# Kernel optimization log

Measured on AMD Instinct MI355X. Metric: run time of the kernel, lower is better.

Reference implementation:

```python
import jax, jax.numpy as jnp
import numpy as np

N_NODES = 100000
N_EDGES = 1600000
N_FEAT = 8
N_EFEAT = 4
STATE = 32  # node_state_size
N_GEN = 10000
ITERS = 3


def _fix_max(m):
    # TF unsorted_segment_max fills empty segments with dtype.min (finite)
    return jnp.where(jnp.isneginf(m), jnp.finfo(m.dtype).min, m)


def _fix_min(m):
    return jnp.where(jnp.isposinf(m), jnp.finfo(m.dtype).max, m)


def _l2_normalize(x, eps=1e-12):
    return x * jax.lax.rsqrt(jnp.maximum(jnp.sum(x * x, axis=-1, keepdims=True), eps))


def _dense_init(key, fan_in, fan_out):
    return jax.random.normal(key, (fan_in, fan_out), jnp.float32) * (1.0 / np.sqrt(fan_in))


def setup_inputs() -> dict:
    key = jax.random.key(0)
    ks = jax.random.split(key, 12)
    x = jax.random.normal(ks[0], (N_NODES, N_FEAT), jnp.float32)
    edge_weights = jax.random.uniform(ks[1], (N_EDGES, N_EFEAT), jnp.float32)
    edges = jax.random.randint(ks[2], (2, N_EDGES), 0, N_NODES)
    generators_nodes = jax.random.randint(ks[3], (N_GEN,), 0, N_NODES)
    # update_fn: 128 -> 256 -> 128 -> 32 (tanh)
    Wu1 = _dense_init(ks[4], 4 * STATE, 256); bu1 = jnp.zeros((256,), jnp.float32)
    Wu2 = _dense_init(ks[5], 256, 128);       bu2 = jnp.zeros((128,), jnp.float32)
    Wu3 = _dense_init(ks[6], 128, STATE);     bu3 = jnp.zeros((STATE,), jnp.float32)
    # readout: 32 -> 64 -> 32 -> 1 (tanh, tanh, linear)
    Wr1 = _dense_init(ks[7], STATE, 64);      br1 = jnp.zeros((64,), jnp.float32)
    Wr2 = _dense_init(ks[8], 64, 32);         br2 = jnp.zeros((32,), jnp.float32)
    Wr3 = _dense_init(ks[9], 32, 1);          br3 = jnp.zeros((1,), jnp.float32)
    return {"x": x, "edge_weights": edge_weights,
            "Wu1": Wu1, "bu1": bu1, "Wu2": Wu2, "bu2": bu2, "Wu3": Wu3, "bu3": bu3,
            "Wr1": Wr1, "br1": br1, "Wr2": Wr2, "br2": br2, "Wr3": Wr3, "br3": br3,
            "edges": edges, "generators_nodes": generators_nodes}


def reference(x, edge_weights, Wu1, bu1, Wu2, bu2, Wu3, bu3,
              Wr1, br1, Wr2, br2, Wr3, br3, edges, generators_nodes):
    n = x.shape[0]
    node_idx, nbr_idx = edges[0], edges[1]
    ones = jnp.ones((edge_weights.shape[0], 1), x.dtype)
    cnt = jnp.maximum(jax.ops.segment_sum(ones, node_idx, num_segments=n), 1.0)  # [n,1]

    # prepare(): edge-weight stats per destination node, concat with features, pad to STATE
    w_sum = jax.ops.segment_sum(edge_weights, node_idx, num_segments=n)
    w_mean = w_sum / cnt
    w_max = _fix_max(jax.ops.segment_max(edge_weights, node_idx, num_segments=n))
    w_min = _fix_min(jax.ops.segment_min(edge_weights, node_idx, num_segments=n))
    reps = jnp.concatenate([x, w_mean, w_max, w_min, w_sum], axis=1)  # [n, 24]
    reps = jnp.pad(reps, ((0, 0), (0, STATE - reps.shape[1])))        # [n, 32]

    for _ in range(ITERS):
        msgs = jnp.take(reps, nbr_idx, axis=0)  # gather neighbour states [E, 32]
        m_mean = jax.ops.segment_sum(msgs, node_idx, num_segments=n) / cnt
        m_max = _fix_max(jax.ops.segment_max(msgs, node_idx, num_segments=n))
        m_min = _fix_min(jax.ops.segment_min(msgs, node_idx, num_segments=n))
        h = jnp.concatenate([reps, m_mean, m_max, m_min], axis=1)  # [n, 128]
        h = jnp.tanh(h @ Wu1 + bu1)
        h = jnp.tanh(h @ Wu2 + bu2)
        h = jnp.tanh(h @ Wu3 + bu3)
        reps = _l2_normalize(h)

    reps = jnp.where(jnp.isnan(reps), jnp.zeros_like(reps), reps)
    g = jnp.take(reps, generators_nodes, axis=0)  # [n_gen, 32]
    g = jnp.tanh(g @ Wr1 + br1)
    g = jnp.tanh(g @ Wr2 + br2)
    values = g @ Wr3 + br3  # linear final activation
    return values.reshape(-1)
```

## Files before the change

### kernel.cpp

```cpp
#include <hip/hip_runtime.h>
#include <cfloat>
#include <cmath>


typedef _Float16 half_t;
typedef _Float16 half8 __attribute__((ext_vector_type(8)));
typedef _Float16 half4_t __attribute__((ext_vector_type(4)));
typedef _Float16 half2_t __attribute__((ext_vector_type(2)));
typedef float f32x4 __attribute__((ext_vector_type(4)));

#define NPB 512
#define BIN_CAP 9216
#define IDXCAP 4352

__device__ __forceinline__ float fast_tanh(float x) {
    float e = __builtin_amdgcn_exp2f(x * 2.8853900817779268f);
    return 1.0f - 2.0f * __builtin_amdgcn_rcpf(1.0f + e);
}

__device__ __forceinline__ half_t cvt_clamp(float v) {
    return (half_t)fminf(fmaxf(v, -60000.f), 60000.f);
}

__device__ __forceinline__ half2_t h2shfl_xor(half2_t v, int mask) {
    int i = __builtin_bit_cast(int, v);
    i = __shfl_xor(i, mask);
    return __builtin_bit_cast(half2_t, i);
}

__global__ __launch_bounds__(256) void k_binA(
    const int* __restrict__ dst, const int* __restrict__ src,
    const float4* __restrict__ ew4,
    int* __restrict__ binCnt, int4* __restrict__ staged, int E, int nbins) {
    __shared__ int cnt[256], base[256], cur[256];
    int t = threadIdx.x;
    cnt[t] = 0;
    cur[t] = 0;
    __syncthreads();
    int e0 = blockIdx.x * 8192;
#pragma unroll 4
    for (int i = 0; i < 32; ++i) {
        int e = e0 + i * 256 + t;
        if (e < E) atomicAdd(&cnt[dst[e] >> 9], 1);
    }
    __syncthreads();
    if (t < nbins && cnt[t] > 0) base[t] = atomicAdd(&binCnt[t], cnt[t]);
    __syncthreads();
#pragma unroll 4
    for (int i = 0; i < 32; ++i) {
        int e = e0 + i * 256 + t;
        if (e < E) {
            int d = dst[e];
            int b = d >> 9;
            int j = base[b] + atomicAdd(&cur[b], 1);
            if (j < BIN_CAP) {
                float4 w = ew4[e];
                half2_t lo = {(half_t)w.x, (half_t)w.y};
                half2_t hi = {(half_t)w.z, (half_t)w.w};
                staged[(size_t)b * BIN_CAP + j] =
                    make_int4(src[e], d & (NPB - 1),
                              __builtin_bit_cast(int, lo),
                              __builtin_bit_cast(int, hi));
            }
        }
    }
}

__global__ void k_scanN(const int* __restrict__ binCnt, int* __restrict__ binStart,
                        int* __restrict__ row_start, int nbins, int n, int E) {
    __shared__ int sh[256];
    int t = threadIdx.x;
    int v = (t < nbins) ? binCnt[t] : 0;
    sh[t] = v;
    __syncthreads();
    for (int s = 1; s < 256; s <<= 1) {
        int u = (t >= s) ? sh[t - s] : 0;
        __syncthreads();
        sh[t] += u;
        __syncthreads();
    }
    if (t < nbins) binStart[t] = sh[t] - v;
    if (t == 0) row_start[n] = E;
}

__global__ __launch_bounds__(512) void k_binB(
    const int* __restrict__ binCnt, const int* __restrict__ binStart,
    const int4* __restrict__ staged, const float* __restrict__ x,
    int* __restrict__ row_start, int* __restrict__ snbr, int2* __restrict__ sew,
    half_t* __restrict__ reps, int n) {
    __shared__ int deg[NPB], cur[NPB], rsl[NPB];
    int t = threadIdx.x;
    int bin = blockIdx.x;
    int cntE = min(binCnt[bin], BIN_CAP);
    int pbase = binStart[bin];
    const int4* st = staged + (size_t)bin * BIN_CAP;

    deg[t] = 0;
    cur[t] = 0;
    __syncthreads();

    for (int i = t; i < cntE; i += 512)
        atomicAdd(&deg[st[i].y], 1);
    __syncthreads();

    int own = deg[t];
    for (int s = 1; s < NPB; s <<= 1) {
        int u = (t >= s) ? deg[t - s] : 0;
        __syncthreads();
        deg[t] += u;
        __syncthreads();
    }
    int excl = deg[t] - own;
    rsl[t] = pbase + excl;
    int node = bin * NPB + t;
    if (node < n) row_start[node] = pbase + excl;
    __syncthreads();

    for (int i = t; i < cntE; i += 512) {
        int4 v = st[i];
        int p = rsl[v.y] + atomicAdd(&cur[v.y], 1);
        snbr[p] = v.x;
        sew[p] = make_int2(v.z, v.w);
    }
    __syncthreads();

    if (node < n) {
        int base = rsl[t];
        float s0 = 0.f, s1 = 0.f, s2 = 0.f, s3 = 0.f;
        half2_t mxlo = {(half_t)-65504.f, (half_t)-65504.f};
        half2_t mxhi = mxlo;
        half2_t mnlo = {(half_t)65504.f, (half_t)65504.f};
        half2_t mnhi = mnlo;
#pragma unroll 2
        for (int k = 0; k < own; ++k) {
            int2 e = sew[base + k];
            half2_t lo = __builtin_bit_cast(half2_t, e.x);
            half2_t hi = __builtin_bit_cast(half2_t, e.y);
            s0 += (float)lo[0];
            s1 += (float)lo[1];
            s2 += (float)hi[0];
            s3 += (float)hi[1];
            mxlo = __builtin_elementwise_max(mxlo, lo);
            mxhi = __builtin_elementwise_max(mxhi, hi);
            mnlo = __builtin_elementwise_min(mnlo, lo);
            mnhi = __builtin_elementwise_min(mnhi, hi);
        }
        float cnt = fmaxf((float)own, 1.0f);
        float rc = __builtin_amdgcn_rcpf(cnt);
        float mx0, mx1, mx2, mx3, mn0, mn1, mn2, mn3;
        if (own == 0) {
            mx0 = mx1 = mx2 = mx3 = -FLT_MAX;
            mn0 = mn1 = mn2 = mn3 = FLT_MAX;
        } else {
            mx0 = (float)mxlo[0]; mx1 = (float)mxlo[1];
            mx2 = (float)mxhi[0]; mx3 = (float)mxhi[1];
            mn0 = (float)mnlo[0]; mn1 = (float)mnlo[1];
            mn2 = (float)mnhi[0]; mn3 = (float)mnhi[1];
        }
        const float4* x4 = reinterpret_cast<const float4*>(x);
        float4 x0 = x4[node * 2 + 0], x1 = x4[node * 2 + 1];
        half_t* o = &reps[(size_t)node * 32];
        half8 c0 = {cvt_clamp(x0.x), cvt_clamp(x0.y), cvt_clamp(x0.z), cvt_clamp(x0.w),
                    cvt_clamp(x1.x), cvt_clamp(x1.y), cvt_clamp(x1.z), cvt_clamp(x1.w)};
        half8 c1 = {cvt_clamp(s0 * rc), cvt_clamp(s1 * rc), cvt_clamp(s2 * rc), cvt_clamp(s3 * rc),
                    cvt_clamp(mx0), cvt_clamp(mx1), cvt_clamp(mx2), cvt_clamp(mx3)};
        half8 c2 = {cvt_clamp(mn0), cvt_clamp(mn1), cvt_clamp(mn2), cvt_clamp(mn3),
                    cvt_clamp(s0), cvt_clamp(s1), cvt_clamp(s2), cvt_clamp(s3)};
        half8 c3 = {(half_t)0.f, (half_t)0.f, (half_t)0.f, (half_t)0.f,
                    (half_t)0.f, (half_t)0.f, (half_t)0.f, (half_t)0.f};
        *(half8*)&o[0] = c0;
        *(half8*)&o[8] = c1;
        *(half8*)&o[16] = c2;
        *(half8*)&o[24] = c3;
    }
}

__global__ void k_wprep(const float* __restrict__ Wu1, const float* __restrict__ Wu2,
                        const float* __restrict__ Wu3, half_t* __restrict__ Wt1,
                        half_t* __restrict__ Wt2, half_t* __restrict__ Wt3) {
    int i = blockIdx.x * 256 + threadIdx.x;
    if (i < 32768) {
        int nrow = i >> 7, k = i & 127;
        Wt1[i] = (half_t)Wu1[k * 256 + nrow];
    } else if (i < 65536) {
        int j = i - 32768;
        int nrow = j >> 8, k = j & 255;
        Wt2[j] = (half_t)Wu2[k * 128 + nrow];
    } else if (i < 69632) {
        int j = i - 65536;
        int nrow = j >> 7, k = j & 127;
        Wt3[j] = (half_t)Wu3[k * 32 + nrow];
    }
}

#define MFMA16(a, b, c) __builtin_amdgcn_mfma_f32_16x16x32_f16((a), (b), (c), 0, 0, 0)

__global__ __launch_bounds__(512, 6) void k_mlp(
    const half_t* __restrict__ reps_in,
    const int* __restrict__ row_start, const int* __restrict__ snbr,
    const int* __restrict__ nlist, int nlen,
    const half_t* __restrict__ Wt1, const half_t* __restrict__ Wt2,
    const half_t* __restrict__ Wt3,
    const float* __restrict__ bu1, const float* __restrict__ bu2,
    const float* __restrict__ bu3,
    half_t* __restrict__ reps_out, int n) {
    __shared__ half_t sH[64 * 136];
    __shared__ half_t sh1c[64 * 136];
    __shared__ int sDeg[64], sPerm[64], sNode[64];
    int* sIdx = (int*)sh1c;

    const int tid = threadIdx.x;
    const int w   = tid >> 6;
    const int l15 = tid & 15;
    const int lk  = (tid & 63) >> 4;
    const int node0 = blockIdx.x * 64;

    if (tid < 64) {
        int node;
        if (nlist) {
            int li = node0 + tid;
            node = (li < nlen) ? nlist[li] : -1;
        } else {
            node = node0 + tid;
        }
        if ((unsigned)node >= (unsigned)n) node = -1;
        sNode[tid] = node;
        sDeg[tid] = (node >= 0) ? (row_start[node + 1] - row_start[node]) : 0;
    }
    const int nodeEnd = min(node0 + 64, n);
    int d0blk = 0;
    bool lds_ok = false;
    if (!nlist && node0 < n) {
        d0blk = row_start[node0];
        int ecnt = row_start[nodeEnd] - d0blk;
        lds_ok = (ecnt <= IDXCAP);
        if (lds_ok) {
            for (int i = tid; i < ecnt; i += 512)
                sIdx[i] = __builtin_nontemporal_load(&snbr[d0blk + i]);
        }
    }
    __syncthreads();
    if (tid < 64) {
        int dg = sDeg[tid];
        int rank = 0;
#pragma unroll
        for (int j = 0; j < 64; ++j) {
            int dj = sDeg[j];
            rank += (dj > dg) || (dj == dg && j < tid);
        }
        sPerm[rank] = tid;
    }
    __syncthreads();

    {
        const int sg = tid >> 4;
        const int l  = tid & 15;
        const int nb = l >> 2;
        const int ch = l & 3;

        for (int i = 0; i < 2; ++i) {
            int nl = sPerm[i * 32 + sg];
            int node = sNode[nl];
            float s[8];
            half2_t mx2[4], mn2[4];
#pragma unroll
            for (int f = 0; f < 8; ++f) s[f] = 0.f;
#pragma unroll
            for (int f = 0; f < 4; ++f) {
                mx2[f] = (half2_t){(half_t)-65504.f, (half_t)-65504.f};
                mn2[f] = (half2_t){(half_t)65504.f, (half_t)65504.f};
            }
            int d0 = 0, d1 = 0;
            if (node >= 0) { d0 = row_start[node]; d1 = row_start[node + 1]; }

            for (int e = d0; e < d1; e += 16) {
                int e0 = e + nb, e1 = e + 4 + nb, e2 = e + 8 + nb, e3 = e + 12 + nb;
                float m0 = (e0 < d1) ? 1.f : 0.f;
                float m1 = (e1 < d1) ? 1.f : 0.f;
                float m2 = (e2 < d1) ? 1.f : 0.f;
                float m3 = (e3 < d1) ? 1.f : 0.f;
                int ii0, ii1, ii2, ii3;
                if (lds_ok) {
                    ii0 = sIdx[min(e0, d1 - 1) - d0blk];
                    ii1 = sIdx[min(e1, d1 - 1) - d0blk];
                    ii2 = sIdx[min(e2, d1 - 1) - d0blk];
                    ii3 = sIdx[min(e3, d1 - 1) - d0blk];
                } else {
                    ii0 = snbr[min(e0, d1 - 1)];
                    ii1 = snbr[min(e1, d1 - 1)];
                    ii2 = snbr[min(e2, d1 - 1)];
                    ii3 = snbr[min(e3, d1 - 1)];
                }
                half8 r0 = *(const half8*)&reps_in[(size_t)ii0 * 32 + ch * 8];
                half8 r1 = *(const half8*)&reps_in[(size_t)ii1 * 32 + ch * 8];
                half8 r2 = *(const half8*)&reps_in[(size_t)ii2 * 32 + ch * 8];
                half8 r3 = *(const half8*)&reps_in[(size_t)ii3 * 32 + ch * 8];
#pragma unroll
                for (int f = 0; f < 4; ++f) {
                    half2_t a0 = (half2_t){r0[2 * f], r0[2 * f + 1]};
                    half2_t a1 = (half2_t){r1[2 * f], r1[2 * f + 1]};
                    half2_t a2 = (half2_t){r2[2 * f], r2[2 * f + 1]};
                    half2_t a3 = (half2_t){r3[2 * f], r3[2 * f + 1]};
                    mx2[f] = __builtin_elementwise_max(
                        __builtin_elementwise_max(mx2[f], a0),
                        __builtin_elementwise_max(a1,
                            __builtin_elementwise_max(a2, a3)));
                    mn2[f] = __builtin_elementwise_min(
                        __builtin_elementwise_min(mn2[f], a0),
                        __builtin_elementwise_min(a1,
                            __builtin_elementwise_min(a2, a3)));
                }
#pragma unroll
                for (int f = 0; f < 8; ++f) {
                    s[f] = fmaf((float)r0[f], m0, s[f]);
                    s[f] = fmaf((float)r1[f], m1, s[f]);
                    s[f] = fmaf((float)r2[f], m2, s[f]);
                    s[f] = fmaf((float)r3[f], m3, s[f]);
                }
            }
#pragma unroll
            for (int f = 0; f < 8; ++f) {
                s[f] += __shfl_xor(s[f], 4);
                s[f] += __shfl_xor(s[f], 8);
            }
#pragma unroll
            for (int f = 0; f < 4; ++f) {
                mx2[f] = __builtin_elementwise_max(mx2[f], h2shfl_xor(mx2[f], 4));
                mx2[f] = __builtin_elementwise_max(mx2[f], h2shfl_xor(mx2[f], 8));
                mn2[f] = __builtin_elementwise_min(mn2[f], h2shfl_xor(mn2[f], 4));
                mn2[f] = __builtin_elementwise_min(mn2[f], h2shfl_xor(mn2[f], 8));
            }
            float cnt = fmaxf((float)(d1 - d0), 1.f);
            half8 o;
            if (nb == 0) {
                if (node >= 0) {
                    o = *(const half8*)&reps_in[(size_t)node * 32 + ch * 8];
                } else {
#pragma unroll
                    for (int f = 0; f < 8; ++f) o[f] = (half_t)0.f;
                }
            } else if (nb == 1) {
                float rc = __builtin_amdgcn_rcpf(cnt);
#pragma unroll
                for (int f = 0; f < 8; ++f) o[f] = cvt_clamp(s[f] * rc);
            } else if (nb == 2) {
#pragma unroll
                for (int f = 0; f < 4; ++f) {
                    o[2 * f]     = cvt_clamp((float)mx2[f][0]);
                    o[2 * f + 1] = cvt_clamp((float)mx2[f][1]);
                }
            } else {
#pragma unroll
                for (int f = 0; f < 4; ++f) {
                    o[2 * f]     = cvt_clamp((float)mn2[f][0]);
                    o[2 * f + 1] = cvt_clamp((float)mn2[f][1]);
                }
            }
            *(half8*)&sH[nl * 136 + l * 8] = o;
        }
    }
    __syncthreads();

    f32x4 acc2[4] = {{0.f, 0.f, 0.f, 0.f}, {0.f, 0.f, 0.f, 0.f},
                     {0.f, 0.f, 0.f, 0.f}, {0.f, 0.f, 0.f, 0.f}};
#pragma unroll
    for (int c = 0; c < 2; ++c) {
        {
            half8 a[4];
#pragma unroll
            for (int ks = 0; ks < 4; ++ks)
                a[ks] = *(const half8*)&Wt1[(c * 128 + w * 16 + l15) * 128 + ks * 32 + lk * 8];
            f32x4 bv = *(const f32x4*)&bu1[c * 128 + w * 16 + lk * 4];
#pragma unroll
            for (int nt = 0; nt < 4; ++nt) {
                const half_t* hrow = &sH[(nt * 16 + l15) * 136 + lk * 8];
                half8 b0 = *(const half8*)&hrow[0];
                half8 b1 = *(const half8*)&hrow[32];
                half8 b2 = *(const half8*)&hrow[64];
                half8 b3 = *(const half8*)&hrow[96];
                f32x4 acc = {0.f, 0.f, 0.f, 0.f};
                acc = MFMA16(a[0], b0, acc);
                acc = MFMA16(a[1], b1, acc);
                acc = MFMA16(a[2], b2, acc);
                acc = MFMA16(a[3], b3, acc);
                half4_t o;
#pragma unroll
                for (int r = 0; r < 4; ++r)
                    o[r] = (half_t)fast_tanh(acc[r] + bv[r]);
                *(half4_t*)&sh1c[(nt * 16 + l15) * 136 + w * 16 + lk * 4] = o;
            }
        }
        __syncthreads();
        {
            half8 a[4];
#pragma unroll
            for (int ks = 0; ks < 4; ++ks)
                a[ks] = *(const half8*)&Wt2[(w * 16 + l15) * 256 + c * 128 + ks * 32 + lk * 8];
#pragma unroll
            for (int nt = 0; nt < 4; ++nt) {
#pragma unroll
                for (int ks = 0; ks < 4; ++ks) {
                    half8 b = *(const half8*)&sh1c[(nt * 16 + l15) * 136 + ks * 32 + lk * 8];
                    acc2[nt] = MFMA16(a[ks], b, acc2[nt]);
                }
            }
        }
        __syncthreads();
    }

    {
        f32x4 bv = *(const f32x4*)&bu2[w * 16 + lk * 4];
#pragma unroll
        for (int nt = 0; nt < 4; ++nt) {
            half4_t o;
#pragma unroll
            for (int r = 0; r < 4; ++r)
                o[r] = (half_t)fast_tanh(acc2[nt][r] + bv[r]);
            *(half4_t*)&sH[(nt * 16 + l15) * 136 + w * 16 + lk * 4] = o;
        }
    }
    __syncthreads();

    if (w < 4) {
        half8 a0[4], a1[4], b[4];
#pragma unroll
        for (int ks = 0; ks < 4; ++ks) {
            a0[ks] = *(const half8*)&Wt3[l15 * 128 + ks * 32 + lk * 8];
            a1[ks] = *(const half8*)&Wt3[(16 + l15) * 128 + ks * 32 + lk * 8];
            b[ks]  = *(const half8*)&sH[(w * 16 + l15) * 136 + ks * 32 + lk * 8];
        }
        f32x4 acc0 = {0.f, 0.f, 0.f, 0.f}, acc1 = {0.f, 0.f, 0.f, 0.f};
#pragma unroll
        for (int ks = 0; ks < 4; ++ks) {
            acc0 = MFMA16(a0[ks], b[ks], acc0);
            acc1 = MFMA16(a1[ks], b[ks], acc1);
        }
        f32x4 bv0 = *(const f32x4*)&bu3[lk * 4];
        f32x4 bv1 = *(const f32x4*)&bu3[16 + lk * 4];
        float v0[4], v1[4];
        float ss = 0.f;
#pragma unroll
        for (int r = 0; r < 4; ++r) {
            v0[r] = fast_tanh(acc0[r] + bv0[r]);
            v1[r] = fast_tanh(acc1[r] + bv1[r]);
            ss += v0[r] * v0[r] + v1[r] * v1[r];
        }
        ss += __shfl_xor(ss, 16);
        ss += __shfl_xor(ss, 32);
        float sc = rsqrtf(fmaxf(ss, 1e-12f));
        int node = sNode[w * 16 + l15];
        if (node >= 0) {
            half4_t o0, o1;
#pragma unroll
            for (int r = 0; r < 4; ++r) {
                o0[r] = (half_t)(v0[r] * sc);
                o1[r] = (half_t)(v1[r] * sc);
            }
            *(half4_t*)&reps_out[(size_t)node * 32 + lk * 4] = o0;
            *(half4_t*)&reps_out[(size_t)node * 32 + 16 + lk * 4] = o1;
        }
    }
}

__global__ __launch_bounds__(256) void k_readout(
    const half_t* __restrict__ reps, const int* __restrict__ gen,
    const float* __restrict__ Wr1, const float* __restrict__ br1,
    const float* __restrict__ Wr2, const float* __restrict__ br2,
    const float* __restrict__ Wr3, const float* __restrict__ br3,
    float* __restrict__ out, int ngen) {
    __shared__ float sW1[32 * 64];
    __shared__ float sW2[64 * 32];
    __shared__ float sb1[64];
    __shared__ float sb2[32];
    __shared__ float sW3r[32];
    __shared__ float sb3;
    int tid = threadIdx.x;
    for (int i = tid; i < 2048; i += 256) sW1[i] = Wr1[i];
    for (int i = tid; i < 2048; i += 256) sW2[i] = Wr2[i];
    if (tid < 64) sb1[tid] = br1[tid];
    if (tid < 32) sb2[tid] = br2[tid];
    if (tid < 32) sW3r[tid] = Wr3[tid];
    if (tid == 0) sb3 = br3[0];
    __syncthreads();
    int ig = blockIdx.x * 256 + tid;
    if (ig >= ngen) return;
    int node = gen[ig];
    float g[32];
#pragma unroll
    for (int q = 0; q < 4; ++q) {
        half8 v = *(const half8*)&reps[(size_t)node * 32 + q * 8];
#pragma unroll
        for (int r = 0; r < 8; ++r) {
            float f = (float)v[r];
            g[q * 8 + r] = (f != f) ? 0.f : f;
        }
    }
    float a[64];
#pragma unroll
    for (int o = 0; o < 64; ++o) {
        float acc = sb1[o];
#pragma unroll
        for (int k = 0; k < 32; ++k) acc = fmaf(g[k], sW1[k * 64 + o], acc);
        a[o] = fast_tanh(acc);
    }
    float b[32];
#pragma unroll
    for (int o = 0; o < 32; ++o) {
        float acc = sb2[o];
#pragma unroll
        for (int k = 0; k < 64; ++k) acc = fmaf(a[k], sW2[k * 32 + o], acc);
        b[o] = fast_tanh(acc);
    }
    float acc = sb3;
#pragma unroll
    for (int k = 0; k < 32; ++k) acc = fmaf(b[k], sW3r[k], acc);
    out[ig] = acc;
}

extern "C" void kernel_launch(void* const* d_in, const int* in_sizes, int n_in,
                              void* d_out, int out_size, void* d_ws, size_t ws_size,
                              hipStream_t stream) {
    const float* x   = (const float*)d_in[0];
    const float* ew  = (const float*)d_in[1];
    const float* Wu1 = (const float*)d_in[2];
    const float* bu1 = (const float*)d_in[3];
    const float* Wu2 = (const float*)d_in[4];
    const float* bu2 = (const float*)d_in[5];
    const float* Wu3 = (const float*)d_in[6];
    const float* bu3 = (const float*)d_in[7];
    const float* Wr1 = (const float*)d_in[8];
    const float* br1 = (const float*)d_in[9];
    const float* Wr2 = (const float*)d_in[10];
    const float* br2 = (const float*)d_in[11];
    const float* Wr3 = (const float*)d_in[12];
    const float* br3 = (const float*)d_in[13];
    const int* edges = (const int*)d_in[14];
    const int* gen   = (const int*)d_in[15];

    const int n    = in_sizes[0] / 8;
    const int E    = in_sizes[1] / 4;
    const int ngen = in_sizes[15];
    const int* dst = edges;
    const int* src = edges + E;
    float* out = (float*)d_out;

    const int nblk  = (n + 63) / 64;
    const int npad  = nblk * 64;
    const int nbins = (n + NPB - 1) / NPB;

    char* ws = (char*)d_ws;
    size_t off = 0;
    auto alloc = [&](size_t bytes) -> char* {
        char* p = ws + off;
        off = (off + bytes + 255) & ~(size_t)255;
        return p;
    };
    int* row_start = (int*)alloc((size_t)(n + 1) * 4);
    int* binCnt    = (int*)alloc(256 * 4);
    int* binStart  = (int*)alloc(256 * 4);
    int* snbr      = (int*)alloc((size_t)E * 4);
    int2* sew      = (int2*)alloc((size_t)E * 8);
    half_t* repsA  = (half_t*)alloc((size_t)npad * 32 * 2);
    half_t* repsB  = (half_t*)alloc((size_t)npad * 32 * 2);
    half_t* Wt1    = (half_t*)alloc(32768 * 2);
    half_t* Wt2    = (half_t*)alloc(32768 * 2);
    half_t* Wt3    = (half_t*)alloc(4096 * 2);
    int4* staged   = (int4*)alloc((size_t)nbins * BIN_CAP * 16);

    hipMemsetAsync(binCnt, 0, 256 * 4, stream);
    int nblkA = (E + 8191) / 8192;
    k_binA<<<nblkA, 256, 0, stream>>>(dst, src, (const float4*)ew, binCnt, staged, E, nbins);
    k_scanN<<<1, 256, 0, stream>>>(binCnt, binStart, row_start, nbins, n, E);
    k_binB<<<nbins, 512, 0, stream>>>(binCnt, binStart, staged, x,
                                      row_start, snbr, sew, repsA, n);
    k_wprep<<<272, 256, 0, stream>>>(Wu1, Wu2, Wu3, Wt1, Wt2, Wt3);

    k_mlp<<<nblk, 512, 0, stream>>>(repsA, row_start, snbr, nullptr, 0,
                                    Wt1, Wt2, Wt3, bu1, bu2, bu3, repsB, n);
    k_mlp<<<nblk, 512, 0, stream>>>(repsB, row_start, snbr, nullptr, 0,
                                    Wt1, Wt2, Wt3, bu1, bu2, bu3, repsA, n);
    int nblk3 = (ngen + 63) / 64;
    k_mlp<<<nblk3, 512, 0, stream>>>(repsA, row_start, snbr, gen, ngen,
                                     Wt1, Wt2, Wt3, bu1, bu2, bu3, repsB, n);

    k_readout<<<(ngen + 255) / 256, 256, 0, stream>>>(repsB, gen, Wr1, br1, Wr2, br2,
                                                      Wr3, br3, out, ngen);
}
```

Measured before the change: 261.8 us.

## Halve k_mlp node tile to 32 with 256-thread blocks and 2x MFMA tiles per wave

Shrinks each k_mlp block from 64 nodes/512 threads to 32 nodes/256 threads, halving shared-memory buffers and the LDS index cap. Each of the four waves now computes two 16-row output tiles per layer, so weight fragments are loaded twice per wave while per-block node work halves. The aim is more, smaller blocks for better load balance and occupancy, at the cost of reloading weights from global/L2 for twice as many blocks.

```diff
diff --git a/kernel.cpp b/kernel.cpp
--- a/kernel.cpp
+++ b/kernel.cpp
@@ -11,7 +11,7 @@
 
 #define NPB 512
 #define BIN_CAP 9216
-#define IDXCAP 4352
+#define IDXCAP 2176
 
 __device__ __forceinline__ float fast_tanh(float x) {
     float e = __builtin_amdgcn_exp2f(x * 2.8853900817779268f);
@@ -195,7 +195,7 @@
 
 #define MFMA16(a, b, c) __builtin_amdgcn_mfma_f32_16x16x32_f16((a), (b), (c), 0, 0, 0)
 
-__global__ __launch_bounds__(512, 6) void k_mlp(
+__global__ __launch_bounds__(256, 6) void k_mlp(
     const half_t* __restrict__ reps_in,
     const int* __restrict__ row_start, const int* __restrict__ snbr,
     const int* __restrict__ nlist, int nlen,
@@ -204,18 +204,18 @@
     const float* __restrict__ bu1, const float* __restrict__ bu2,
     const float* __restrict__ bu3,
     half_t* __restrict__ reps_out, int n) {
-    __shared__ half_t sH[64 * 136];
-    __shared__ half_t sh1c[64 * 136];
-    __shared__ int sDeg[64], sPerm[64], sNode[64];
+    __shared__ half_t sH[32 * 136];
+    __shared__ half_t sh1c[32 * 136];
+    __shared__ int sDeg[32], sPerm[32], sNode[32];
     int* sIdx = (int*)sh1c;
 
     const int tid = threadIdx.x;
     const int w   = tid >> 6;
     const int l15 = tid & 15;
     const int lk  = (tid & 63) >> 4;
-    const int node0 = blockIdx.x * 64;
-
-    if (tid < 64) {
+    const int node0 = blockIdx.x * 32;
+
+    if (tid < 32) {
         int node;
         if (nlist) {
             int li = node0 + tid;
@@ -227,7 +227,7 @@
         sNode[tid] = node;
         sDeg[tid] = (node >= 0) ? (row_start[node + 1] - row_start[node]) : 0;
     }
-    const int nodeEnd = min(node0 + 64, n);
+    const int nodeEnd = min(node0 + 32, n);
     int d0blk = 0;
     bool lds_ok = false;
     if (!nlist && node0 < n) {
@@ -235,16 +235,16 @@
         int ecnt = row_start[nodeEnd] - d0blk;
         lds_ok = (ecnt <= IDXCAP);
         if (lds_ok) {
-            for (int i = tid; i < ecnt; i += 512)
+            for (int i = tid; i < ecnt; i += 256)
                 sIdx[i] = __builtin_nontemporal_load(&snbr[d0blk + i]);
         }
     }
     __syncthreads();
-    if (tid < 64) {
+    if (tid < 32) {
         int dg = sDeg[tid];
         int rank = 0;
 #pragma unroll
-        for (int j = 0; j < 64; ++j) {
+        for (int j = 0; j < 32; ++j) {
             int dj = sDeg[j];
             rank += (dj > dg) || (dj == dg && j < tid);
         }
@@ -259,7 +259,7 @@
         const int ch = l & 3;
 
         for (int i = 0; i < 2; ++i) {
-            int nl = sPerm[i * 32 + sg];
+            int nl = sPerm[i * 16 + sg];
             int node = sNode[nl];
             float s[8];
             half2_t mx2[4], mn2[4];
@@ -361,47 +361,61 @@
     }
     __syncthreads();
 
-    f32x4 acc2[4] = {{0.f, 0.f, 0.f, 0.f}, {0.f, 0.f, 0.f, 0.f},
-                     {0.f, 0.f, 0.f, 0.f}, {0.f, 0.f, 0.f, 0.f}};
+    f32x4 acc2[2][2] = {{{0.f, 0.f, 0.f, 0.f}, {0.f, 0.f, 0.f, 0.f}},
+                        {{0.f, 0.f, 0.f, 0.f}, {0.f, 0.f, 0.f, 0.f}}};
 #pragma unroll
     for (int c = 0; c < 2; ++c) {
         {
-            half8 a[4];
-#pragma unroll
-            for (int ks = 0; ks < 4; ++ks)
-                a[ks] = *(const half8*)&Wt1[(c * 128 + w * 16 + l15) * 128 + ks * 32 + lk * 8];
-            f32x4 bv = *(const f32x4*)&bu1[c * 128 + w * 16 + lk * 4];
-#pragma unroll
-            for (int nt = 0; nt < 4; ++nt) {
+            half8 a0[4], a1[4];
+#pragma unroll
+            for (int ks = 0; ks < 4; ++ks) {
+                a0[ks] = *(const half8*)&Wt1[(c * 128 + w * 32 + l15) * 128 + ks * 32 + lk * 8];
+                a1[ks] = *(const half8*)&Wt1[(c * 128 + w * 32 + 16 + l15) * 128 + ks * 32 + lk * 8];
+            }
+            f32x4 bv0 = *(const f32x4*)&bu1[c * 128 + w * 32 + lk * 4];
+            f32x4 bv1 = *(const f32x4*)&bu1[c * 128 + w * 32 + 16 + lk * 4];
+#pragma unroll
+            for (int nt = 0; nt < 2; ++nt) {
                 const half_t* hrow = &sH[(nt * 16 + l15) * 136 + lk * 8];
                 half8 b0 = *(const half8*)&hrow[0];
                 half8 b1 = *(const half8*)&hrow[32];
                 half8 b2 = *(const half8*)&hrow[64];
                 half8 b3 = *(const half8*)&hrow[96];
-                f32x4 acc = {0.f, 0.f, 0.f, 0.f};
-                acc = MFMA16(a[0], b0, acc);
-                acc = MFMA16(a[1], b1, acc);
-                acc = MFMA16(a[2], b2, acc);
-                acc = MFMA16(a[3], b3, acc);
-                half4_t o;
-#pragma unroll
-                for (int r = 0; r < 4; ++r)
-                    o[r] = (half_t)fast_tanh(acc[r] + bv[r]);
-                *(half4_t*)&sh1c[(nt * 16 + l15) * 136 + w * 16 + lk * 4] = o;
+                f32x4 acc0 = {0.f, 0.f, 0.f, 0.f}, acc1 = {0.f, 0.f, 0.f, 0.f};
+                acc0 = MFMA16(a0[0], b0, acc0);
+                acc0 = MFMA16(a0[1], b1, acc0);
+                acc0 = MFMA16(a0[2], b2, acc0);
+                acc0 = MFMA16(a0[3], b3, acc0);
+                acc1 = MFMA16(a1[0], b0, acc1);
+                acc1 = MFMA16(a1[1], b1, acc1);
+                acc1 = MFMA16(a1[2], b2, acc1);
+                acc1 = MFMA16(a1[3], b3, acc1);
+                int nodeLoc = nt * 16 + l15;
+                half4_t o0, o1;
+#pragma unroll
+                for (int r = 0; r < 4; ++r) {
+                    o0[r] = (half_t)fast_tanh(acc0[r] + bv0[r]);
+                    o1[r] = (half_t)fast_tanh(acc1[r] + bv1[r]);
+                }
+                *(half4_t*)&sh1c[nodeLoc * 136 + w * 32 + lk * 4] = o0;
+                *(half4_t*)&sh1c[nodeLoc * 136 + w * 32 + 16 + lk * 4] = o1;
             }
         }
         __syncthreads();
         {
-            half8 a[4];
-#pragma unroll
-            for (int ks = 0; ks < 4; ++ks)
-                a[ks] = *(const half8*)&Wt2[(w * 16 + l15) * 256 + c * 128 + ks * 32 + lk * 8];
-#pragma unroll
-            for (int nt = 0; nt < 4; ++nt) {
+            half8 aA[4], aB[4];
+#pragma unroll
+            for (int ks = 0; ks < 4; ++ks) {
+                aA[ks] = *(const half8*)&Wt2[(w * 32 + l15) * 256 + c * 128 + ks * 32 + lk * 8];
+                aB[ks] = *(const half8*)&Wt2[(w * 32 + 16 + l15) * 256 + c * 128 + ks * 32 + lk * 8];
+            }
+#pragma unroll
+            for (int nt = 0; nt < 2; ++nt) {
 #pragma unroll
                 for (int ks = 0; ks < 4; ++ks) {
                     half8 b = *(const half8*)&sh1c[(nt * 16 + l15) * 136 + ks * 32 + lk * 8];
-                    acc2[nt] = MFMA16(a[ks], b, acc2[nt]);
+                    acc2[0][nt] = MFMA16(aA[ks], b, acc2[0][nt]);
+                    acc2[1][nt] = MFMA16(aB[ks], b, acc2[1][nt]);
                 }
             }
         }
@@ -409,19 +423,23 @@
     }
 
     {
-        f32x4 bv = *(const f32x4*)&bu2[w * 16 + lk * 4];
-#pragma unroll
-        for (int nt = 0; nt < 4; ++nt) {
-            half4_t o;
-#pragma unroll
-            for (int r = 0; r < 4; ++r)
-                o[r] = (half_t)fast_tanh(acc2[nt][r] + bv[r]);
-            *(half4_t*)&sH[(nt * 16 + l15) * 136 + w * 16 + lk * 4] = o;
-        }
-    }
-    __syncthreads();
-
-    if (w < 4) {
+        f32x4 bv0 = *(const f32x4*)&bu2[w * 32 + lk * 4];
+        f32x4 bv1 = *(const f32x4*)&bu2[w * 32 + 16 + lk * 4];
+#pragma unroll
+        for (int nt = 0; nt < 2; ++nt) {
+            half4_t o0, o1;
+#pragma unroll
+            for (int r = 0; r < 4; ++r) {
+                o0[r] = (half_t)fast_tanh(acc2[0][nt][r] + bv0[r]);
+                o1[r] = (half_t)fast_tanh(acc2[1][nt][r] + bv1[r]);
+            }
+            *(half4_t*)&sH[(nt * 16 + l15) * 136 + w * 32 + lk * 4] = o0;
+            *(half4_t*)&sH[(nt * 16 + l15) * 136 + w * 32 + 16 + lk * 4] = o1;
+        }
+    }
+    __syncthreads();
+
+    if (w < 2) {
         half8 a0[4], a1[4], b[4];
 #pragma unroll
         for (int ks = 0; ks < 4; ++ks) {
@@ -544,8 +562,8 @@
     const int* src = edges + E;
     float* out = (float*)d_out;
 
-    const int nblk  = (n + 63) / 64;
-    const int npad  = nblk * 64;
+    const int nblk  = (n + 31) / 32;
+    const int npad  = nblk * 32;
     const int nbins = (n + NPB - 1) / NPB;
 
     char* ws = (char*)d_ws;
@@ -575,12 +593,12 @@
                                       row_start, snbr, sew, repsA, n);
     k_wprep<<<272, 256, 0, stream>>>(Wu1, Wu2, Wu3, Wt1, Wt2, Wt3);
 
-    k_mlp<<<nblk, 512, 0, stream>>>(repsA, row_start, snbr, nullptr, 0,
+    k_mlp<<<nblk, 256, 0, stream>>>(repsA, row_start, snbr, nullptr, 0,
                                     Wt1, Wt2, Wt3, bu1, bu2, bu3, repsB, n);
-    k_mlp<<<nblk, 512, 0, stream>>>(repsB, row_start, snbr, nullptr, 0,
+    k_mlp<<<nblk, 256, 0, stream>>>(repsB, row_start, snbr, nullptr, 0,
                                     Wt1, Wt2, Wt3, bu1, bu2, bu3, repsA, n);
-    int nblk3 = (ngen + 63) / 64;
-    k_mlp<<<nblk3, 512, 0, stream>>>(repsA, row_start, snbr, gen, ngen,
+    int nblk3 = (ngen + 31) / 32;
+    k_mlp<<<nblk3, 256, 0, stream>>>(repsA, row_start, snbr, gen, ngen,
                                      Wt1, Wt2, Wt3, bu1, bu2, bu3, repsB, n);
 
     k_readout<<<(ngen + 255) / 256, 256, 0, stream>>>(repsB, gen, Wr1, br1, Wr2, br2,
```

Result: slower. 296.1 us (+13.1%).
